# Performance work log

Measured on AMD Instinct MI355X. Metric: run time of the kernel, lower is better.

## Reference

```python
import jax, jax.numpy as jnp
import numpy as np

B, S, HID = 4, 4096, 2048
H, G = 16, 4
D = HID // H  # head_dim = 128
KV = HID * G // H  # k/v proj out dim = 512


def setup_inputs() -> dict:
    key = jax.random.key(0)
    ks = jax.random.split(key, 9)
    s = lambda fan_in: 1.0 / np.sqrt(fan_in)
    return {
        "hidden_states": jax.random.normal(ks[0], (B, S, HID), jnp.float32),
        "Wq": jax.random.uniform(ks[1], (HID, HID), jnp.float32, -s(HID), s(HID)),
        "bq": jnp.zeros((HID,), jnp.float32),
        "Wk": jax.random.uniform(ks[2], (HID, KV), jnp.float32, -s(HID), s(HID)),
        "bk": jnp.zeros((KV,), jnp.float32),
        "Wv": jax.random.uniform(ks[3], (HID, KV), jnp.float32, -s(HID), s(HID)),
        "bv": jnp.zeros((KV,), jnp.float32),
        "Wo": jax.random.uniform(ks[4], (HID, HID), jnp.float32, -s(HID), s(HID)),
        "bo": jnp.zeros((HID,), jnp.float32),
    }


def reference(hidden_states, Wq, bq, Wk, bk, Wv, bv, Wo, bo):
    # Projections (torch Linear: x @ W^T + b; here W stored as [in, out])
    q = hidden_states @ Wq + bq            # [B,S,HID]
    k = hidden_states @ Wk + bk            # [B,S,KV]
    v = hidden_states @ Wv + bv            # [B,S,KV]
    q = q.reshape(B, S, H, D)
    k = k.reshape(B, S, G, D)
    v = v.reshape(B, S, G, D)
    # Faithful to source: scores over groups at the SAME position, [B,S,H,G]
    scores = jnp.einsum("bshd,bsgd->bshg", q, k) / jnp.sqrt(jnp.float32(D))
    probs = jax.nn.softmax(scores, axis=-1)  # softmax over G
    out = jnp.einsum("bshg,bsgd->bshd", probs, v)  # [B,S,H,D]
    out = out.reshape(B, S, HID)
    return out @ Wo + bo
```

## Files before the change

### kernel.cpp

```cpp
#include <hip/hip_runtime.h>
#include <hip/hip_bf16.h>
#include <stdint.h>

typedef __bf16 bf16_t;
typedef __bf16 bf16x8 __attribute__((ext_vector_type(8)));
typedef __bf16 bf16x4_t __attribute__((ext_vector_type(4)));
typedef float f32x4 __attribute__((ext_vector_type(4)));

#define AS1 __attribute__((address_space(1)))
#define AS3 __attribute__((address_space(3)))

__device__ __forceinline__ void stage16(const bf16_t* g, char* l) {
    __builtin_amdgcn_global_load_lds((const AS1 uint32_t*)g, (AS3 uint32_t*)l, 16, 0, 0);
}

#define BAR()   __builtin_amdgcn_s_barrier()
#define LGKM0() asm volatile("s_waitcnt lgkmcnt(0)" ::: "memory")
#define VMC(N)  asm volatile("s_waitcnt vmcnt(" #N ")" ::: "memory")
#define PRIO(p) __builtin_amdgcn_s_setprio(p)

template <typename OutT>
__global__ __launch_bounds__(512, 2) void gemm256(
    const bf16_t* __restrict__ A, int lda,
    const bf16_t* __restrict__ Bt, int ldb,
    const float* __restrict__ bias,
    OutT* __restrict__ C, int ldc,
    int K, int nTilesN)
{
    __shared__ char smem[131072];
    const int tid  = threadIdx.x;
    const int wave = tid >> 6;
    const int lane = tid & 63;
    const int wm = wave >> 2;
    const int wn = wave & 3;

    const int bid = blockIdx.x;
    const int swz = (bid & 7) * ((int)gridDim.x >> 3) + (bid >> 3);
    const int m0 = (swz / nTilesN) << 8;
    const int n0 = (swz % nTilesN) << 8;

    const int srow = lane >> 2;
    const int scol = ((lane & 3) * 8) ^ ((lane & 32) >> 1);
    const bf16_t* aS0 = A  + (size_t)(m0 + wave * 32 + srow) * lda + scol;
    const bf16_t* aS1 = aS0 + (size_t)16 * lda;
    const bf16_t* bS0 = Bt + (size_t)(n0 + wave * 32 + srow) * ldb + scol;
    const bf16_t* bS1 = bS0 + (size_t)16 * ldb;

#define STAGE_A(b,kk,kb) do { \
    stage16(aS0 + (kb) + (kk)*32, smem + (b)*65536 + (kk)*16384 + wave*2048); \
    stage16(aS1 + (kb) + (kk)*32, smem + (b)*65536 + (kk)*16384 + wave*2048 + 1024); } while(0)
#define STAGE_B(b,kk,kb) do { \
    stage16(bS0 + (kb) + (kk)*32, smem + (b)*65536 + 32768 + (kk)*16384 + wave*2048); \
    stage16(bS1 + (kb) + (kk)*32, smem + (b)*65536 + 32768 + (kk)*16384 + wave*2048 + 1024); } while(0)

    const int rdLane = (lane & 15) * 64 + (((lane >> 4) * 16) ^ ((lane & 8) << 2));
    const char* aRdB = smem + rdLane + wm * 8192;
    const char* bRdB = smem + 32768 + rdLane + wn * 4096;

    f32x4 acc[8][4];
#pragma unroll
    for (int i = 0; i < 8; ++i)
#pragma unroll
        for (int j = 0; j < 4; ++j) acc[i][j] = (f32x4){0.f, 0.f, 0.f, 0.f};
    bf16x8 bfr[2][4];
    bf16x8 af[2][2];

#define RDB8(b) { _Pragma("unroll") \
    for (int kk = 0; kk < 2; ++kk) _Pragma("unroll") \
        for (int ni = 0; ni < 4; ++ni) \
            bfr[kk][ni] = *(const bf16x8*)(bRdB + (b)*65536 + kk*16384 + ni*1024); }
#define RDA(b,mp) { _Pragma("unroll") \
    for (int t = 0; t < 2; ++t) _Pragma("unroll") \
        for (int kk = 0; kk < 2; ++kk) \
            af[t][kk] = *(const bf16x8*)(aRdB + (b)*65536 + kk*16384 + ((mp)*2+t)*1024); }
#define MF(mp) { _Pragma("unroll") \
    for (int t = 0; t < 2; ++t) _Pragma("unroll") \
        for (int ni = 0; ni < 4; ++ni) _Pragma("unroll") \
            for (int kk = 0; kk < 2; ++kk) \
                acc[(mp)*2+t][ni] = __builtin_amdgcn_mfma_f32_16x16x32_bf16(af[t][kk], bfr[kk][ni], acc[(mp)*2+t][ni], 0, 0, 0); }
#define PH(STG, RDS, WAIT, MFM) do { \
    STG; RDS; WAIT; LGKM0(); BAR(); PRIO(1); MFM; PRIO(0); } while(0)

    STAGE_A(0, 0, 0);  STAGE_A(0, 1, 0);  STAGE_B(0, 0, 0);  STAGE_B(0, 1, 0);
    STAGE_B(1, 0, 64); STAGE_B(1, 1, 64);
    VMC(0);
    BAR();

    const int NI = K >> 7;
    for (int it = 0; it < NI - 1; ++it) {
        const int kB  = (it << 7) + 64;
        const int kN0 = (it << 7) + 128;
        const int kN1 = (it << 7) + 192;
        PH(STAGE_A(1,0,kB); STAGE_A(1,1,kB), RDB8(0); RDA(0,0), , MF(0));
        PH(STAGE_B(0,0,kN0),                 RDA(0,1),          , MF(1));
        PH(STAGE_B(0,1,kN0),                 RDA(0,2),          , MF(2));
        PH(,                                 RDA(0,3),    VMC(4), MF(3));
        PH(STAGE_A(0,0,kN0),                 RDB8(1); RDA(1,0), , MF(0));
        PH(STAGE_A(0,1,kN0),                 RDA(1,1),          , MF(1));
        PH(STAGE_B(1,0,kN1),                 RDA(1,2),          , MF(2));
        PH(STAGE_B(1,1,kN1),                 RDA(1,3),    VMC(4), MF(3));
    }
    {
        const int kB = ((NI - 1) << 7) + 64;
        PH(STAGE_A(1,0,kB); STAGE_A(1,1,kB), RDB8(0); RDA(0,0), , MF(0));
        PH(,                                 RDA(0,1),          , MF(1));
        PH(,                                 RDA(0,2),          , MF(2));
        PH(,                                 RDA(0,3),    VMC(0), MF(3));
        PH(,                                 RDB8(1); RDA(1,0), , MF(0));
        PH(,                                 RDA(1,1),          , MF(1));
        PH(,                                 RDA(1,2),          , MF(2));
        PH(,                                 RDA(1,3),          , MF(3));
    }
    BAR();

    {
        const int mrow = lane & 15;
        const int quad = lane >> 4;
        constexpr int CSZ = (int)sizeof(OutT);
        float bias_v[4];
#pragma unroll
        for (int ni = 0; ni < 4; ++ni)
            bias_v[ni] = bias[n0 + wn * 64 + ni * 16 + mrow];
#pragma unroll
        for (int h = 0; h < 2; ++h) {
            if (wm == h) {
#pragma unroll
                for (int ni = 0; ni < 4; ++ni) {
                    const int colb = (wn * 64 + ni * 16 + mrow) * CSZ;
#pragma unroll
                    for (int mi = 0; mi < 8; ++mi)
#pragma unroll
                        for (int r = 0; r < 4; ++r) {
                            const int lrow = mi * 16 + quad * 4 + r;
                            *(OutT*)(smem + lrow * 256 * CSZ + (colb ^ (quad * 16 * CSZ))) =
                                (OutT)(acc[mi][ni][r] + bias_v[ni]);
                        }
                }
            }
            BAR();
            const int ROUNDS = 128 * 256 * CSZ / 8192;
#pragma unroll
            for (int rd = 0; rd < ROUNDS; ++rd) {
                const int flat = rd * 8192 + tid * 16;
                const int lrow = flat / (256 * CSZ);
                const int colb = flat % (256 * CSZ);
                const int q2 = (lrow >> 2) & 3;
                uint4 v = *(const uint4*)(smem + lrow * 256 * CSZ + (colb ^ (q2 * 16 * CSZ)));
                *(uint4*)((char*)C + ((size_t)(m0 + h * 128 + lrow) * ldc + n0) * CSZ + colb) = v;
            }
            BAR();
        }
    }
#undef STAGE_A
#undef STAGE_B
#undef RDB8
#undef RDA
#undef MF
#undef PH
}

__global__ __launch_bounds__(256) void f32_to_bf16(const float* __restrict__ src,
                                                   bf16_t* __restrict__ dst, int n4) {
    int i = blockIdx.x * 256 + threadIdx.x;
    if (i >= n4) return;
    float4 v = ((const float4*)src)[i];
    bf16x4_t o;
    o.x = (bf16_t)v.x; o.y = (bf16_t)v.y; o.z = (bf16_t)v.z; o.w = (bf16_t)v.w;
    ((bf16x4_t*)dst)[i] = o;
}

__global__ __launch_bounds__(256) void transpose_convert(
    const float* __restrict__ src, bf16_t* __restrict__ dst,
    int rows, int cols)
{
    __shared__ bf16_t t[64][65];
    const int tx = threadIdx.x & 63;
    const int ty = threadIdx.x >> 6;
    const int c0 = blockIdx.x * 64;
    const int r0 = blockIdx.y * 64;
#pragma unroll
    for (int r = ty; r < 64; r += 4)
        t[r][tx] = (bf16_t)src[(size_t)(r0 + r) * cols + c0 + tx];
    __syncthreads();
#pragma unroll
    for (int r = ty; r < 64; r += 4)
        dst[(size_t)(c0 + r) * rows + r0 + tx] = t[tx][r];
}

__global__ void concat_bias(const float* __restrict__ bq, const float* __restrict__ bk,
                            const float* __restrict__ bv, float* __restrict__ o) {
    int i = blockIdx.x * 256 + threadIdx.x;
    if (i >= 3072) return;
    o[i] = (i < 2048) ? bq[i] : (i < 2560 ? bk[i - 2048] : bv[i - 2560]);
}

__global__ __launch_bounds__(256) void gqa_attn(
    const bf16_t* __restrict__ q, int sq,
    const bf16_t* __restrict__ kv, int skv,
    bf16_t* __restrict__ out, int so)
{
    const int token = blockIdx.x;
    const int wave = threadIdx.x >> 6, lane = threadIdx.x & 63;
    const bf16_t* qb  = q  + (size_t)token * sq;
    const bf16_t* kvb = kv + (size_t)token * skv;
    const float scale = 0.08838834764831845f;
    float k0[4], k1[4], v0[4], v1[4];
#pragma unroll
    for (int g = 0; g < 4; ++g) {
        uint32_t ku = *(const uint32_t*)(kvb + g * 128 + lane * 2);
        k0[g] = __uint_as_float(ku << 16);
        k1[g] = __uint_as_float(ku & 0xffff0000u);
        uint32_t vu = *(const uint32_t*)(kvb + 512 + g * 128 + lane * 2);
        v0[g] = __uint_as_float(vu << 16);
        v1[g] = __uint_as_float(vu & 0xffff0000u);
    }
#pragma unroll
    for (int hh = 0; hh < 4; ++hh) {
        const int h = wave * 4 + hh;
        uint32_t qu = *(const uint32_t*)(qb + h * 128 + lane * 2);
        float q0 = __uint_as_float(qu << 16);
        float q1 = __uint_as_float(qu & 0xffff0000u);
        float s[4];
#pragma unroll
        for (int g = 0; g < 4; ++g) s[g] = q0 * k0[g] + q1 * k1[g];
#pragma unroll
        for (int off = 32; off > 0; off >>= 1)
#pragma unroll
            for (int g = 0; g < 4; ++g) s[g] += __shfl_xor(s[g], off);
        float mx = fmaxf(fmaxf(s[0], s[1]), fmaxf(s[2], s[3]));
        float e[4], sum = 0.f;
#pragma unroll
        for (int g = 0; g < 4; ++g) { e[g] = __expf((s[g] - mx) * scale); sum += e[g]; }
        const float rs = 1.0f / sum;
        float o0 = 0.f, o1 = 0.f;
#pragma unroll
        for (int g = 0; g < 4; ++g) { o0 += e[g] * v0[g]; o1 += e[g] * v1[g]; }
        o0 *= rs; o1 *= rs;
        bf16_t* op = out + (size_t)token * so + h * 128 + lane * 2;
        op[0] = (bf16_t)o0;
        op[1] = (bf16_t)o1;
    }
}

extern "C" void kernel_launch(void* const* d_in, const int* in_sizes, int n_in,
                              void* d_out, int out_size, void* d_ws, size_t ws_size,
                              hipStream_t stream) {
    const float* hs = (const float*)d_in[0];
    const float* Wq = (const float*)d_in[1];
    const float* bq = (const float*)d_in[2];
    const float* Wk = (const float*)d_in[3];
    const float* bk = (const float*)d_in[4];
    const float* Wv = (const float*)d_in[5];
    const float* bv = (const float*)d_in[6];
    const float* Wo = (const float*)d_in[7];
    const float* bo = (const float*)d_in[8];
    float* outp = (float*)d_out;
    char* ws = (char*)d_ws;

    bf16_t* Wt     = (bf16_t*)(ws);
    bf16_t* Wot    = (bf16_t*)(ws + 12582912);
    float*  bqkv   = (float*)(ws + 20971520);
    bf16_t* hs_b   = (bf16_t*)(ws + 20983808);
    bf16_t* atto   = (bf16_t*)(ws + 20983808);
    bf16_t* qkv    = (bf16_t*)d_out;

    f32_to_bf16<<<32768, 256, 0, stream>>>(hs, hs_b, 8388608);
    transpose_convert<<<dim3(32, 32), 256, 0, stream>>>(Wq, Wt, 2048, 2048);
    transpose_convert<<<dim3(8, 32), 256, 0, stream>>>(Wk, Wt + (size_t)2048 * 2048, 2048, 512);
    transpose_convert<<<dim3(8, 32), 256, 0, stream>>>(Wv, Wt + (size_t)2560 * 2048, 2048, 512);
    transpose_convert<<<dim3(32, 32), 256, 0, stream>>>(Wo, Wot, 2048, 2048);
    concat_bias<<<12, 256, 0, stream>>>(bq, bk, bv, bqkv);

    gemm256<bf16_t><<<768, 512, 0, stream>>>(hs_b, 2048, Wt, 2048, bqkv, qkv, 3072, 2048, 12);
    gqa_attn<<<16384, 256, 0, stream>>>(qkv, 3072, qkv + 2048, 3072, atto, 2048);
    gemm256<float><<<512, 512, 0, stream>>>(atto, 2048, Wot, 2048, bo, outp, 2048, 2048, 8);
}
```

Before: 638.1 us.

## Double-buffer LDS fragment registers to overlap reads with MFMA in GEMM

Splits the A and B LDS fragment registers into ping-pong buffers, so the reads for the next phase are issued before the current phase's MFMAs run, rather than waiting on them first. The phase order is changed to barrier, read, stage, MFMA, then wait, and the vmcnt thresholds are adjusted to match. The aim is to hide LDS read latency behind matrix math, at the cost of roughly double the fragment registers, which may pressure occupancy at 2 blocks per CU. Barrier placement relative to the async LDS staging writes also changes, which risks a race if the wait counts are wrong.

```diff
diff --git a/kernel.cpp b/kernel.cpp
--- a/kernel.cpp
+++ b/kernel.cpp
@@ -62,54 +62,55 @@
     for (int i = 0; i < 8; ++i)
 #pragma unroll
         for (int j = 0; j < 4; ++j) acc[i][j] = (f32x4){0.f, 0.f, 0.f, 0.f};
-    bf16x8 bfr[2][4];
-    bf16x8 af[2][2];
-
-#define RDB8(b) { _Pragma("unroll") \
+    bf16x8 bA[2][2][2];
+    bf16x8 bB[2][2][4];
+
+#define RDB8S(b,s) { _Pragma("unroll") \
     for (int kk = 0; kk < 2; ++kk) _Pragma("unroll") \
         for (int ni = 0; ni < 4; ++ni) \
-            bfr[kk][ni] = *(const bf16x8*)(bRdB + (b)*65536 + kk*16384 + ni*1024); }
-#define RDA(b,mp) { _Pragma("unroll") \
+            bB[s][kk][ni] = *(const bf16x8*)(bRdB + (b)*65536 + kk*16384 + ni*1024); }
+#define RDAP(b,mp,pa) { _Pragma("unroll") \
     for (int t = 0; t < 2; ++t) _Pragma("unroll") \
         for (int kk = 0; kk < 2; ++kk) \
-            af[t][kk] = *(const bf16x8*)(aRdB + (b)*65536 + kk*16384 + ((mp)*2+t)*1024); }
-#define MF(mp) { _Pragma("unroll") \
+            bA[pa][t][kk] = *(const bf16x8*)(aRdB + (b)*65536 + kk*16384 + ((mp)*2+t)*1024); }
+#define MFP(mp,pa,s) { _Pragma("unroll") \
     for (int t = 0; t < 2; ++t) _Pragma("unroll") \
         for (int ni = 0; ni < 4; ++ni) _Pragma("unroll") \
             for (int kk = 0; kk < 2; ++kk) \
-                acc[(mp)*2+t][ni] = __builtin_amdgcn_mfma_f32_16x16x32_bf16(af[t][kk], bfr[kk][ni], acc[(mp)*2+t][ni], 0, 0, 0); }
-#define PH(STG, RDS, WAIT, MFM) do { \
-    STG; RDS; WAIT; LGKM0(); BAR(); PRIO(1); MFM; PRIO(0); } while(0)
+                acc[(mp)*2+t][ni] = __builtin_amdgcn_mfma_f32_16x16x32_bf16(bA[pa][t][kk], bB[s][kk][ni], acc[(mp)*2+t][ni], 0, 0, 0); }
+#define PH(RDS, STG, MFM, WAIT) do { \
+    BAR(); RDS; STG; PRIO(1); MFM; PRIO(0); WAIT; LGKM0(); } while(0)
 
     STAGE_A(0, 0, 0);  STAGE_A(0, 1, 0);  STAGE_B(0, 0, 0);  STAGE_B(0, 1, 0);
     STAGE_B(1, 0, 64); STAGE_B(1, 1, 64);
     VMC(0);
     BAR();
+    RDB8S(0, 0); RDAP(0, 0, 1); LGKM0();
 
     const int NI = K >> 7;
     for (int it = 0; it < NI - 1; ++it) {
         const int kB  = (it << 7) + 64;
         const int kN0 = (it << 7) + 128;
         const int kN1 = (it << 7) + 192;
-        PH(STAGE_A(1,0,kB); STAGE_A(1,1,kB), RDB8(0); RDA(0,0), , MF(0));
-        PH(STAGE_B(0,0,kN0),                 RDA(0,1),          , MF(1));
-        PH(STAGE_B(0,1,kN0),                 RDA(0,2),          , MF(2));
-        PH(,                                 RDA(0,3),    VMC(4), MF(3));
-        PH(STAGE_A(0,0,kN0),                 RDB8(1); RDA(1,0), , MF(0));
-        PH(STAGE_A(0,1,kN0),                 RDA(1,1),          , MF(1));
-        PH(STAGE_B(1,0,kN1),                 RDA(1,2),          , MF(2));
-        PH(STAGE_B(1,1,kN1),                 RDA(1,3),    VMC(4), MF(3));
+        PH(RDAP(0,1,0),              STAGE_A(1,0,kB); STAGE_A(1,1,kB), MFP(0,1,0), );
+        PH(RDAP(0,2,1),              STAGE_B(0,0,kN0),                 MFP(1,0,0), );
+        PH(RDAP(0,3,0),              STAGE_B(0,1,kN0),                 MFP(2,1,0), VMC(4));
+        PH(RDB8S(1,1); RDAP(1,0,1),  ,                                 MFP(3,0,0), );
+        PH(RDAP(1,1,0),              STAGE_A(0,0,kN0),                 MFP(0,1,1), );
+        PH(RDAP(1,2,1),              STAGE_A(0,1,kN0),                 MFP(1,0,1), );
+        PH(RDAP(1,3,0),              STAGE_B(1,0,kN1),                 MFP(2,1,1), VMC(2));
+        PH(RDB8S(0,0); RDAP(0,0,1),  STAGE_B(1,1,kN1),                 MFP(3,0,1), );
     }
     {
         const int kB = ((NI - 1) << 7) + 64;
-        PH(STAGE_A(1,0,kB); STAGE_A(1,1,kB), RDB8(0); RDA(0,0), , MF(0));
-        PH(,                                 RDA(0,1),          , MF(1));
-        PH(,                                 RDA(0,2),          , MF(2));
-        PH(,                                 RDA(0,3),    VMC(0), MF(3));
-        PH(,                                 RDB8(1); RDA(1,0), , MF(0));
-        PH(,                                 RDA(1,1),          , MF(1));
-        PH(,                                 RDA(1,2),          , MF(2));
-        PH(,                                 RDA(1,3),          , MF(3));
+        PH(RDAP(0,1,0),              STAGE_A(1,0,kB); STAGE_A(1,1,kB), MFP(0,1,0), );
+        PH(RDAP(0,2,1),              ,                                 MFP(1,0,0), );
+        PH(RDAP(0,3,0),              ,                                 MFP(2,1,0), VMC(0));
+        PH(RDB8S(1,1); RDAP(1,0,1),  ,                                 MFP(3,0,0), );
+        PH(RDAP(1,1,0),              ,                                 MFP(0,1,1), );
+        PH(RDAP(1,2,1),              ,                                 MFP(1,0,1), );
+        PH(RDAP(1,3,0),              ,                                 MFP(2,1,1), );
+        BAR(); PRIO(1); MFP(3,0,1); PRIO(0);
     }
     BAR();
 
@@ -153,9 +154,9 @@
     }
 #undef STAGE_A
 #undef STAGE_B
-#undef RDB8
-#undef RDA
-#undef MF
+#undef RDB8S
+#undef RDAP
+#undef MFP
 #undef PH
 }
 
```

New measurement: 640.4 us. About the same (+0.4%).

## Remap GQA attention to one thread per (token, head) with vectorized loads

Applied to the files above, without the earlier changes.

Reworks the per-token group attention kernel so that each thread handles a whole (token, head) pair instead of spreading a head across a wave. Each thread computes its dot products serially over 16-byte vector loads, which removes the cross-lane shuffle reductions. The launch grid shrinks from one block per token to one block per 16 tokens. The trade-offs are strided, less coalesced global accesses across threads, with K/V re-read by every head thread (cache-dependent), and more registers per thread.

```diff
diff --git a/kernel.cpp b/kernel.cpp
--- a/kernel.cpp
+++ b/kernel.cpp
@@ -195,50 +195,59 @@
 }
 
 __global__ __launch_bounds__(256) void gqa_attn(
-    const bf16_t* __restrict__ q, int sq,
-    const bf16_t* __restrict__ kv, int skv,
+    const bf16_t* __restrict__ qkv, int sq,
     bf16_t* __restrict__ out, int so)
 {
-    const int token = blockIdx.x;
-    const int wave = threadIdx.x >> 6, lane = threadIdx.x & 63;
-    const bf16_t* qb  = q  + (size_t)token * sq;
-    const bf16_t* kvb = kv + (size_t)token * skv;
+    const int t = blockIdx.x * 256 + threadIdx.x;
+    const int token = t >> 4;
+    const int h = t & 15;
+    const bf16_t* qb = qkv + (size_t)token * sq + h * 128;
+    const bf16_t* kb = qkv + (size_t)token * sq + 2048;
+    const bf16_t* vb = kb + 512;
     const float scale = 0.08838834764831845f;
-    float k0[4], k1[4], v0[4], v1[4];
-#pragma unroll
-    for (int g = 0; g < 4; ++g) {
-        uint32_t ku = *(const uint32_t*)(kvb + g * 128 + lane * 2);
-        k0[g] = __uint_as_float(ku << 16);
-        k1[g] = __uint_as_float(ku & 0xffff0000u);
-        uint32_t vu = *(const uint32_t*)(kvb + 512 + g * 128 + lane * 2);
-        v0[g] = __uint_as_float(vu << 16);
-        v1[g] = __uint_as_float(vu & 0xffff0000u);
-    }
-#pragma unroll
-    for (int hh = 0; hh < 4; ++hh) {
-        const int h = wave * 4 + hh;
-        uint32_t qu = *(const uint32_t*)(qb + h * 128 + lane * 2);
-        float q0 = __uint_as_float(qu << 16);
-        float q1 = __uint_as_float(qu & 0xffff0000u);
-        float s[4];
-#pragma unroll
-        for (int g = 0; g < 4; ++g) s[g] = q0 * k0[g] + q1 * k1[g];
-#pragma unroll
-        for (int off = 32; off > 0; off >>= 1)
-#pragma unroll
-            for (int g = 0; g < 4; ++g) s[g] += __shfl_xor(s[g], off);
-        float mx = fmaxf(fmaxf(s[0], s[1]), fmaxf(s[2], s[3]));
-        float e[4], sum = 0.f;
-#pragma unroll
-        for (int g = 0; g < 4; ++g) { e[g] = __expf((s[g] - mx) * scale); sum += e[g]; }
-        const float rs = 1.0f / sum;
-        float o0 = 0.f, o1 = 0.f;
-#pragma unroll
-        for (int g = 0; g < 4; ++g) { o0 += e[g] * v0[g]; o1 += e[g] * v1[g]; }
-        o0 *= rs; o1 *= rs;
-        bf16_t* op = out + (size_t)token * so + h * 128 + lane * 2;
-        op[0] = (bf16_t)o0;
-        op[1] = (bf16_t)o1;
+
+    float s[4] = {0.f, 0.f, 0.f, 0.f};
+#pragma unroll 4
+    for (int c = 0; c < 16; ++c) {
+        const uint4 qv = *(const uint4*)(qb + c * 8);
+        const uint32_t qa[4] = {qv.x, qv.y, qv.z, qv.w};
+#pragma unroll
+        for (int g = 0; g < 4; ++g) {
+            const uint4 kv4 = *(const uint4*)(kb + g * 128 + c * 8);
+            const uint32_t ka[4] = {kv4.x, kv4.y, kv4.z, kv4.w};
+#pragma unroll
+            for (int w = 0; w < 4; ++w) {
+                s[g] += __uint_as_float(qa[w] << 16) * __uint_as_float(ka[w] << 16);
+                s[g] += __uint_as_float(qa[w] & 0xffff0000u) * __uint_as_float(ka[w] & 0xffff0000u);
+            }
+        }
+    }
+    const float mx = fmaxf(fmaxf(s[0], s[1]), fmaxf(s[2], s[3]));
+    float p[4], sum = 0.f;
+#pragma unroll
+    for (int g = 0; g < 4; ++g) { p[g] = __expf((s[g] - mx) * scale); sum += p[g]; }
+    const float rs = 1.0f / sum;
+#pragma unroll
+    for (int g = 0; g < 4; ++g) p[g] *= rs;
+
+    bf16_t* ob = out + (size_t)token * so + h * 128;
+#pragma unroll 4
+    for (int c = 0; c < 16; ++c) {
+        float o0[8] = {0.f, 0.f, 0.f, 0.f, 0.f, 0.f, 0.f, 0.f};
+#pragma unroll
+        for (int g = 0; g < 4; ++g) {
+            const uint4 vv = *(const uint4*)(vb + g * 128 + c * 8);
+            const uint32_t va[4] = {vv.x, vv.y, vv.z, vv.w};
+#pragma unroll
+            for (int w = 0; w < 4; ++w) {
+                o0[w * 2]     += p[g] * __uint_as_float(va[w] << 16);
+                o0[w * 2 + 1] += p[g] * __uint_as_float(va[w] & 0xffff0000u);
+            }
+        }
+        bf16x8 ov;
+#pragma unroll
+        for (int j = 0; j < 8; ++j) ov[j] = (bf16_t)o0[j];
+        *(bf16x8*)(ob + c * 8) = ov;
     }
 }
 
@@ -272,6 +281,6 @@
     concat_bias<<<12, 256, 0, stream>>>(bq, bk, bv, bqkv);
 
     gemm256<bf16_t><<<768, 512, 0, stream>>>(hs_b, 2048, Wt, 2048, bqkv, qkv, 3072, 2048, 12);
-    gqa_attn<<<16384, 256, 0, stream>>>(qkv, 3072, qkv + 2048, 3072, atto, 2048);
+    gqa_attn<<<1024, 256, 0, stream>>>(qkv, 3072, atto, 2048);
     gemm256<float><<<512, 512, 0, stream>>>(atto, 2048, Wot, 2048, bo, outp, 2048, 2048, 8);
 }
```

Measured after the change: 613.1 us. 1.04x faster.
